# Kernel tuning notes

Measured on AMD Instinct MI355X. Metric: run time of the kernel, lower is better.

## Reference

```python
import jax, jax.numpy as jnp
import numpy as np

N_NODES = 100000
N_EDGES = 1600000
IN_F = 128
HEADS = 4
D_K = 32
OUT_TOTAL = HEADS * D_K


def setup_inputs() -> dict:
    key = jax.random.key(0)
    k1, k2, k3, k4, k5, k6 = jax.random.split(key, 6)
    x = jax.random.normal(k1, (N_NODES, IN_F), dtype=jnp.float32)
    edge_index = jax.random.randint(k2, (2, N_EDGES), 0, N_NODES, dtype=jnp.int64)
    # torch nn.Linear weights: [out, in], xavier-uniform init
    def xavier(k, shape):
        fan_out, fan_in = shape
        lim = float(np.sqrt(6.0 / (fan_in + fan_out)))
        return jax.random.uniform(k, shape, dtype=jnp.float32, minval=-lim, maxval=lim)
    Wq = xavier(k3, (OUT_TOTAL, IN_F))
    Wk = xavier(k4, (OUT_TOTAL, IN_F))
    Wv = xavier(k5, (OUT_TOTAL, IN_F))
    # D init_type='uniform': U(-1, 1)
    D = jax.random.uniform(k6, (HEADS, D_K), dtype=jnp.float32, minval=-1.0, maxval=1.0)
    return {"x": x, "Wq": Wq, "Wk": Wk, "Wv": Wv, "D": D, "edge_index": edge_index}


def reference(x, Wq, Wk, Wv, D, edge_index):
    N = x.shape[0]
    scale = 1.0 / np.sqrt(D_K)
    Q = (x @ Wq.T).reshape(N, HEADS, D_K)
    K = (x @ Wk.T).reshape(N, HEADS, D_K)
    V = (x @ Wv.T).reshape(N, HEADS, D_K)
    row, col = edge_index[0], edge_index[1]
    K_i = K[row]              # [E, H, d]
    Q_j = Q[col]              # [E, H, d]
    diff = K_i - Q_j
    # non-self edges: diff^T diag(D) diff ; self edges: K^T diag(D) Q
    score_edge = jnp.sum(diff * D * diff, axis=-1)          # [E, H]
    score_self = jnp.sum(K_i * D * Q[row], axis=-1)         # [E, H]
    self_mask = (row == col)[:, None]
    scores = jnp.where(self_mask, score_self, score_edge)
    scores = jax.nn.leaky_relu(scores * scale, 0.2)
    # segment softmax over destination node `row`
    smax = jax.ops.segment_max(scores, row, num_segments=N)  # [N, H]
    ex = jnp.exp(scores - smax[row])
    ssum = jax.ops.segment_sum(ex, row, num_segments=N)      # [N, H]
    alpha = ex / (ssum[row] + 1e-16)
    # scatter-add aggregate alpha * V[col] into destination rows
    out = jax.ops.segment_sum(alpha[:, :, None] * V[col], row, num_segments=N)
    return out.reshape(N, OUT_TOTAL)
```

## Files before the change

### kernel.cpp

```cpp
#include <hip/hip_runtime.h>
#include <hip/hip_fp16.h>
#include <cmath>


#define HEADS 4
#define DK 32
#define FDIM 128
#define BINSHIFT 8
#define BINCAP 6144

typedef _Float16 f16x8 __attribute__((ext_vector_type(8)));
typedef float f32x4 __attribute__((ext_vector_type(4)));

__global__ __launch_bounds__(256) void init_buffers(
    int* __restrict__ bin_cursor, int nb)
{
    int gid = blockIdx.x * 256 + threadIdx.x;
    if (gid < nb) bin_cursor[gid] = 0;
}

__global__ __launch_bounds__(256) void split_w(
    const float* __restrict__ Wq, const float* __restrict__ Wk,
    const float* __restrict__ Wv, _Float16* __restrict__ Whf,
    _Float16* __restrict__ Wlf)
{
    const int p = blockIdx.x;
    const float* __restrict__ W = (p == 0) ? Wq : (p == 1 ? Wk : Wv);
#pragma unroll
    for (int i = 0; i < 8; ++i) {
        const int id = i * 256 + threadIdx.x;
        const int g  = id >> 8;
        const int kc = (id >> 6) & 3;
        const int l  = id & 63;
        const int row  = g * 16 + (l & 15);
        const int col0 = kc * 32 + (l >> 4) * 8;
        const float* src = W + row * FDIM + col0;
        const float4 v0 = *reinterpret_cast<const float4*>(src);
        const float4 v1 = *reinterpret_cast<const float4*>(src + 4);
        const float vv[8] = {v0.x, v0.y, v0.z, v0.w, v1.x, v1.y, v1.z, v1.w};
        f16x8 h, lo;
#pragma unroll
        for (int j = 0; j < 8; ++j) {
            _Float16 hh = (_Float16)vv[j];
            h[j]  = hh;
            lo[j] = (_Float16)(vv[j] - (float)hh);
        }
        const size_t off = ((size_t)((p * 8 + g) * 4 + kc) * 64 + l) * 8;
        *reinterpret_cast<f16x8*>(Whf + off) = h;
        *reinterpret_cast<f16x8*>(Wlf + off) = lo;
    }
}

__global__ __launch_bounds__(256) void partition_edges(
    const int* __restrict__ row, const int* __restrict__ col,
    int* __restrict__ bin_cursor, unsigned* __restrict__ pairs,
    int E, int N, int NB)
{
    __shared__ int hist[512];
    __shared__ int basea[512];
    __shared__ int cura[512];
    const int tid = threadIdx.x;
    for (int b = tid; b < 512; b += 256) { hist[b] = 0; cura[b] = 0; }
    __syncthreads();

    const int e0 = blockIdx.x * 4096;
    int rr[16], cc[16];
    if (e0 + 4096 <= E) {
#pragma unroll
        for (int i = 0; i < 4; ++i) {
            const int idx = e0 + i * 1024 + tid * 4;
            const int4 r4 = *reinterpret_cast<const int4*>(row + idx);
            const int4 c4 = *reinterpret_cast<const int4*>(col + idx);
            rr[i*4+0] = r4.x; rr[i*4+1] = r4.y; rr[i*4+2] = r4.z; rr[i*4+3] = r4.w;
            cc[i*4+0] = c4.x; cc[i*4+1] = c4.y; cc[i*4+2] = c4.z; cc[i*4+3] = c4.w;
        }
    } else {
#pragma unroll
        for (int i = 0; i < 4; ++i)
#pragma unroll
            for (int j = 0; j < 4; ++j) {
                const int idx = e0 + i * 1024 + tid * 4 + j;
                rr[i*4+j] = (idx < E) ? row[idx] : -1;
                cc[i*4+j] = (idx < E) ? col[idx] : 0;
            }
    }

#pragma unroll
    for (int i = 0; i < 16; ++i)
        if ((unsigned)rr[i] < (unsigned)N)
            atomicAdd(&hist[rr[i] >> BINSHIFT], 1);
    __syncthreads();

    for (int b = tid; b < NB; b += 256) {
        const int h = hist[b];
        basea[b] = h ? atomicAdd(&bin_cursor[b], h) : 0;
    }
    __syncthreads();

#pragma unroll
    for (int i = 0; i < 16; ++i) {
        const int r = rr[i];
        if ((unsigned)r < (unsigned)N) {
            const int b = r >> BINSHIFT;
            const int p = basea[b] + atomicAdd(&cura[b], 1);
            if (p < BINCAP)
                pairs[(size_t)b * BINCAP + p] =
                    (unsigned)(r & 255) | ((unsigned)cc[i] << 8);
        }
    }
}

__global__ __launch_bounds__(256) void build_csr(
    const int* __restrict__ bin_cursor, const unsigned* __restrict__ pairs,
    int* __restrict__ csr, int* __restrict__ offA, int* __restrict__ cntA,
    int N)
{
    __shared__ int deg[256];
    __shared__ int offs[256];
    __shared__ int cur[256];
    const int b = blockIdx.x;
    const int tid = threadIdx.x;
    deg[tid] = 0;
    __syncthreads();

    int nsize = bin_cursor[b];
    if (nsize > BINCAP) nsize = BINCAP;
    const unsigned* bp = pairs + (size_t)b * BINCAP;

    for (int i = tid; i < nsize; i += 256)
        atomicAdd(&deg[bp[i] & 255], 1);
    __syncthreads();

    const int v = deg[tid];
    offs[tid] = v;
    __syncthreads();
    for (int o = 1; o < 256; o <<= 1) {
        const int t = (tid >= o) ? offs[tid - o] : 0;
        __syncthreads();
        offs[tid] += t;
        __syncthreads();
    }
    const int excl = offs[tid] - v;
    cur[tid] = excl;
    const int node = (b << BINSHIFT) + tid;
    if (node < N) {
        offA[node] = b * BINCAP + excl;
        cntA[node] = v;
    }
    __syncthreads();

    for (int i = tid; i < nsize; i += 256) {
        const unsigned pv = bp[i];
        const int p = atomicAdd(&cur[pv & 255], 1);
        csr[(size_t)b * BINCAP + p] = (int)(pv >> 8);
    }
}

__device__ __forceinline__ int swz_idx(int row, int kk) {
    return (row * FDIM + kk) ^ ((row & 7) << 3);
}

__device__ __forceinline__ void stage_x(
    const float* __restrict__ src, _Float16* __restrict__ dh,
    _Float16* __restrict__ dl, int n0, int nmax, int tid)
{
    const int kk0 = (tid & 15) * 8;
    const int r0  = tid >> 4;
#pragma unroll
    for (int i = 0; i < 4; ++i) {
        const int row = i * 16 + r0;
        float4 v0 = make_float4(0.f, 0.f, 0.f, 0.f), v1 = v0;
        if (n0 + row < nmax) {
            const float* p = src + (size_t)(n0 + row) * FDIM + kk0;
            v0 = *reinterpret_cast<const float4*>(p);
            v1 = *reinterpret_cast<const float4*>(p + 4);
        }
        const float vv[8] = {v0.x, v0.y, v0.z, v0.w, v1.x, v1.y, v1.z, v1.w};
        f16x8 h, l;
#pragma unroll
        for (int j = 0; j < 8; ++j) {
            _Float16 hh = (_Float16)vv[j];
            h[j] = hh;
            l[j] = (_Float16)(vv[j] - (float)hh);
        }
        const int si = swz_idx(row, kk0);
        *reinterpret_cast<f16x8*>(&dh[si]) = h;
        *reinterpret_cast<f16x8*>(&dl[si]) = l;
    }
}

__global__ __launch_bounds__(256) void qkv_gemm(
    const float* __restrict__ x, const _Float16* __restrict__ Whf,
    const _Float16* __restrict__ Wlf, __half* __restrict__ QVh,
    float* __restrict__ Kout, int N)
{
    __shared__ __align__(16) _Float16 xh[64 * 128];
    __shared__ __align__(16) _Float16 xl[64 * 128];

    const int n0  = blockIdx.x * 64;
    const int tid = threadIdx.x;
    const int lane = tid & 63;
    const int wv   = tid >> 6;
    const int wr0  = (wv >> 1) * 32;
    const int wc0  = (wv & 1) * 64;
    const int g0   = wc0 >> 4;
    const int orow = (lane >> 4) * 4;
    const int ocol = lane & 15;

    stage_x(x, xh, xl, n0, N, tid);
    __syncthreads();

    const int lrow = lane & 15;
    const int lk   = (lane >> 4) * 8;

    for (int p = 0; p < 3; ++p) {
        f32x4 acc[2][4];
#pragma unroll
        for (int a = 0; a < 2; ++a)
#pragma unroll
            for (int b = 0; b < 4; ++b)
                acc[a][b] = (f32x4){0.f, 0.f, 0.f, 0.f};

#pragma unroll
        for (int kc = 0; kc < 4; ++kc) {
            f16x8 afh[2], afl[2], bfh[4], bfl[4];
#pragma unroll
            for (int a = 0; a < 2; ++a) {
                const int si = swz_idx(wr0 + a * 16 + lrow, kc * 32 + lk);
                afh[a] = *reinterpret_cast<const f16x8*>(&xh[si]);
                afl[a] = *reinterpret_cast<const f16x8*>(&xl[si]);
            }
#pragma unroll
            for (int b = 0; b < 4; ++b) {
                const size_t off =
                    ((size_t)((p * 8 + g0 + b) * 4 + kc) * 64 + lane) * 8;
                bfh[b] = *reinterpret_cast<const f16x8*>(Whf + off);
                bfl[b] = *reinterpret_cast<const f16x8*>(Wlf + off);
            }
#pragma unroll
            for (int a = 0; a < 2; ++a)
#pragma unroll
                for (int b = 0; b < 4; ++b)
                    acc[a][b] = __builtin_amdgcn_mfma_f32_16x16x32_f16(
                        afh[a], bfh[b], acc[a][b], 0, 0, 0);
#pragma unroll
            for (int a = 0; a < 2; ++a)
#pragma unroll
                for (int b = 0; b < 4; ++b)
                    acc[a][b] = __builtin_amdgcn_mfma_f32_16x16x32_f16(
                        afl[a], bfh[b], acc[a][b], 0, 0, 0);
#pragma unroll
            for (int a = 0; a < 2; ++a)
#pragma unroll
                for (int b = 0; b < 4; ++b)
                    acc[a][b] = __builtin_amdgcn_mfma_f32_16x16x32_f16(
                        afh[a], bfl[b], acc[a][b], 0, 0, 0);
        }

        if (p == 1) {
#pragma unroll
            for (int a = 0; a < 2; ++a) {
#pragma unroll
                for (int r = 0; r < 4; ++r) {
                    const int n = n0 + wr0 + a * 16 + orow + r;
                    if (n < N) {
                        float* op = Kout + (size_t)n * FDIM + wc0 + ocol;
#pragma unroll
                        for (int b = 0; b < 4; ++b)
                            op[b * 16] = acc[a][b][r];
                    }
                }
            }
        } else {
            const int voff = (p == 2) ? 2 : 0;
#pragma unroll
            for (int a = 0; a < 2; ++a) {
#pragma unroll
                for (int r = 0; r < 4; ++r) {
                    const int n = n0 + wr0 + a * 16 + orow + r;
                    if (n < N) {
                        __half* op = QVh + (size_t)n * 256;
#pragma unroll
                        for (int b = 0; b < 4; ++b) {
                            const int d_o = wc0 + ocol + b * 16;
                            op[((d_o >> 1) << 2) + (d_o & 1) + voff] =
                                __float2half(acc[a][b][r]);
                        }
                    }
                }
            }
        }
    }
}

__global__ __launch_bounds__(256) void fused_aggregate(
    const int* __restrict__ offA, const int* __restrict__ cntA,
    const int* __restrict__ csr, const __half* __restrict__ QVh,
    const float* Kb, const float* __restrict__ D, float* out, int N)
{
    int node = blockIdx.x * 4 + (threadIdx.x >> 6);
    if (node >= N) return;
    int lane = threadIdx.x & 63;
    int d = lane * 2;
    const float2 kv = *reinterpret_cast<const float2*>(Kb + (size_t)node * FDIM + d);
    const float D0 = D[d], D1 = D[d + 1];
    const int j0  = offA[node];
    const int cnt = cntA[node];
    float a0 = 0.0f, a1 = 0.0f, se = 0.0f;

    int cc0, cc1, cc2, cc3;
    float2 t0, t1, t2, t3;

#define LOADF(s, idx) { int c_ = __shfl(ec, (idx)); cc##s = c_; \
    t##s = *reinterpret_cast<const float2*>( \
        reinterpret_cast<const __half*>(QVh) + (size_t)c_ * 256 + (lane << 2)); }

#define PROC(s) { \
    float2 qf = __half22float2(*reinterpret_cast<__half2*>(&t##s.x)); \
    float2 vf = __half22float2(*reinterpret_cast<__half2*>(&t##s.y)); \
    float p; \
    if (cc##s == node) { p = D0 * kv.x * qf.x + D1 * kv.y * qf.y; } \
    else { float dx = kv.x - qf.x, dy = kv.y - qf.y; \
           p = D0 * dx * dx + D1 * dy * dy; } \
    p += __shfl_xor(p, 1); p += __shfl_xor(p, 2); \
    p += __shfl_xor(p, 4); p += __shfl_xor(p, 8); \
    float z = p * 0.17677669529663687f; \
    z = fmaxf(z, 0.2f * z); \
    float ex = __expf(z); \
    a0 += ex * vf.x; a1 += ex * vf.y; se += ex; }

    for (int base = 0; base < cnt; base += 64) {
        const int rem = min(64, cnt - base);
        const int ec = (lane < rem) ? csr[j0 + base + lane] : 0;
        int j = 0;
        if (rem >= 4) {
            LOADF(0, 0) LOADF(1, 1) LOADF(2, 2) LOADF(3, 3)
            while (j + 8 <= rem) {
                PROC(0) LOADF(0, j + 4)
                PROC(1) LOADF(1, j + 5)
                PROC(2) LOADF(2, j + 6)
                PROC(3) LOADF(3, j + 7)
                j += 4;
            }
            PROC(0) PROC(1) PROC(2) PROC(3)
            j += 4;
        }
        for (; j < rem; ++j) {
            LOADF(0, j)
            PROC(0)
        }
    }
#undef LOADF
#undef PROC

    float inv = 1.0f / (se + 1e-16f);
    *reinterpret_cast<float2*>(out + (size_t)node * FDIM + d) =
        make_float2(a0 * inv, a1 * inv);
}

extern "C" void kernel_launch(void* const* d_in, const int* in_sizes, int n_in,
                              void* d_out, int out_size, void* d_ws, size_t ws_size,
                              hipStream_t stream) {
    const float* x  = (const float*)d_in[0];
    const float* Wq = (const float*)d_in[1];
    const float* Wk = (const float*)d_in[2];
    const float* Wv = (const float*)d_in[3];
    const float* D  = (const float*)d_in[4];
    const int*  edge = (const int*)d_in[5];
    float* out = (float*)d_out;

    const int N = in_sizes[0] / FDIM;
    const int E = in_sizes[5] / 2;
    const int* row = edge;
    const int* col = edge + E;

    const int NB = (N + 255) >> 8;

    __half* QVh = (__half*)d_ws;
    unsigned* pairs = (unsigned*)(QVh + (size_t)N * 256);
    int* csr  = (int*)(pairs + (size_t)NB * BINCAP);
    int* offA = csr + (size_t)NB * BINCAP;
    int* cntA = offA + N;
    int* bin_cursor = cntA + N;
    _Float16* Whf = (_Float16*)(bin_cursor + 512);
    _Float16* Wlf = Whf + 3 * 16384;
    float* Kout = out;

    init_buffers<<<(NB + 255) / 256, 256, 0, stream>>>(bin_cursor, NB);
    split_w<<<3, 256, 0, stream>>>(Wq, Wk, Wv, Whf, Wlf);

    partition_edges<<<(E + 4095) / 4096, 256, 0, stream>>>(
        row, col, bin_cursor, pairs, E, N, NB);
    build_csr<<<NB, 256, 0, stream>>>(
        bin_cursor, pairs, csr, offA, cntA, N);

    qkv_gemm<<<(N + 63) / 64, 256, 0, stream>>>(
        x, Whf, Wlf, QVh, Kout, N);

    fused_aggregate<<<(N + 3) / 4, 256, 0, stream>>>(
        offA, cntA, csr, QVh, Kout, D, out, N);
}
```

Measured before the change: 314.5 us.

## Process two edges per wave with 16-byte QV gathers in aggregation

The fp16 Q/V buffer is re-interleaved in groups of four dims, so each lane loads 4 Q plus 4 V values in one 16-byte load. Each half-wave now handles a separate edge, so a wave covers two edges per step, and the two halves' accumulators are merged at the end. The CSR now stores precomputed byte offsets (node<<9) to save address arithmetic. The head reduction drops to three shuffles, and an odd trailing edge is split half-weight across both halves. Separately, the tiny init_buffers kernel is folded into split_w to save a launch.

```diff
diff --git a/kernel.cpp b/kernel.cpp
--- a/kernel.cpp
+++ b/kernel.cpp
@@ -12,18 +12,14 @@
 typedef _Float16 f16x8 __attribute__((ext_vector_type(8)));
 typedef float f32x4 __attribute__((ext_vector_type(4)));
 
-__global__ __launch_bounds__(256) void init_buffers(
-    int* __restrict__ bin_cursor, int nb)
-{
-    int gid = blockIdx.x * 256 + threadIdx.x;
-    if (gid < nb) bin_cursor[gid] = 0;
-}
-
 __global__ __launch_bounds__(256) void split_w(
     const float* __restrict__ Wq, const float* __restrict__ Wk,
     const float* __restrict__ Wv, _Float16* __restrict__ Whf,
-    _Float16* __restrict__ Wlf)
-{
+    _Float16* __restrict__ Wlf, int* __restrict__ bin_cursor, int nb)
+{
+    const int gid = blockIdx.x * 256 + threadIdx.x;
+    if (gid < nb) bin_cursor[gid] = 0;
+
     const int p = blockIdx.x;
     const float* __restrict__ W = (p == 0) ? Wq : (p == 1 ? Wk : Wv);
 #pragma unroll
@@ -152,7 +148,7 @@
     for (int i = tid; i < nsize; i += 256) {
         const unsigned pv = bp[i];
         const int p = atomicAdd(&cur[pv & 255], 1);
-        csr[(size_t)b * BINCAP + p] = (int)(pv >> 8);
+        csr[(size_t)b * BINCAP + p] = (int)((pv >> 8) << 9);
     }
 }
 
@@ -272,7 +268,7 @@
                 }
             }
         } else {
-            const int voff = (p == 2) ? 2 : 0;
+            const int voff = (p == 2) ? 4 : 0;
 #pragma unroll
             for (int a = 0; a < 2; ++a) {
 #pragma unroll
@@ -283,7 +279,7 @@
 #pragma unroll
                         for (int b = 0; b < 4; ++b) {
                             const int d_o = wc0 + ocol + b * 16;
-                            op[((d_o >> 1) << 2) + (d_o & 1) + voff] =
+                            op[((d_o >> 2) << 3) + (d_o & 3) + voff] =
                                 __float2half(acc[a][b][r]);
                         }
                     }
@@ -300,62 +296,101 @@
 {
     int node = blockIdx.x * 4 + (threadIdx.x >> 6);
     if (node >= N) return;
-    int lane = threadIdx.x & 63;
-    int d = lane * 2;
-    const float2 kv = *reinterpret_cast<const float2*>(Kb + (size_t)node * FDIM + d);
-    const float D0 = D[d], D1 = D[d + 1];
+    const int lane = threadIdx.x & 63;
+    const int hl   = lane & 31;
+    const int side = lane >> 5;
+    const int d0   = hl << 2;
+    const float4 kv = *reinterpret_cast<const float4*>(Kb + (size_t)node * FDIM + d0);
+    const float4 Dv = *reinterpret_cast<const float4*>(D + d0);
+    const float Dk0 = Dv.x * kv.x, Dk1 = Dv.y * kv.y,
+                Dk2 = Dv.z * kv.z, Dk3 = Dv.w * kv.w;
     const int j0  = offA[node];
     const int cnt = cntA[node];
-    float a0 = 0.0f, a1 = 0.0f, se = 0.0f;
+    const int nb  = node << 9;
+    float a0 = 0.f, a1 = 0.f, a2 = 0.f, a3 = 0.f, se = 0.f;
 
     int cc0, cc1, cc2, cc3;
-    float2 t0, t1, t2, t3;
-
-#define LOADF(s, idx) { int c_ = __shfl(ec, (idx)); cc##s = c_; \
-    t##s = *reinterpret_cast<const float2*>( \
-        reinterpret_cast<const __half*>(QVh) + (size_t)c_ * 256 + (lane << 2)); }
-
-#define PROC(s) { \
-    float2 qf = __half22float2(*reinterpret_cast<__half2*>(&t##s.x)); \
-    float2 vf = __half22float2(*reinterpret_cast<__half2*>(&t##s.y)); \
+    float4 t0, t1, t2, t3;
+
+#define LOADP(s, p) { int c_ = __shfl(ecb, 2 * (p) + side); cc##s = c_; \
+    t##s = *reinterpret_cast<const float4*>( \
+        reinterpret_cast<const char*>(QVh) + (size_t)(unsigned)c_ + (hl << 4)); }
+
+#define PROCP(s) { \
+    const __half2* th = reinterpret_cast<const __half2*>(&t##s); \
+    float2 q01 = __half22float2(th[0]); float2 q23 = __half22float2(th[1]); \
+    float2 v01 = __half22float2(th[2]); float2 v23 = __half22float2(th[3]); \
     float p; \
-    if (cc##s == node) { p = D0 * kv.x * qf.x + D1 * kv.y * qf.y; } \
-    else { float dx = kv.x - qf.x, dy = kv.y - qf.y; \
-           p = D0 * dx * dx + D1 * dy * dy; } \
-    p += __shfl_xor(p, 1); p += __shfl_xor(p, 2); \
-    p += __shfl_xor(p, 4); p += __shfl_xor(p, 8); \
+    if (cc##s == nb) { \
+        p = Dk0 * q01.x + Dk1 * q01.y + Dk2 * q23.x + Dk3 * q23.y; \
+    } else { \
+        float e0 = kv.x - q01.x, e1 = kv.y - q01.y; \
+        float e2 = kv.z - q23.x, e3 = kv.w - q23.y; \
+        p = Dv.x*e0*e0 + Dv.y*e1*e1 + Dv.z*e2*e2 + Dv.w*e3*e3; \
+    } \
+    p += __shfl_xor(p, 1); p += __shfl_xor(p, 2); p += __shfl_xor(p, 4); \
     float z = p * 0.17677669529663687f; \
     z = fmaxf(z, 0.2f * z); \
     float ex = __expf(z); \
-    a0 += ex * vf.x; a1 += ex * vf.y; se += ex; }
+    a0 += ex * v01.x; a1 += ex * v01.y; \
+    a2 += ex * v23.x; a3 += ex * v23.y; se += ex; }
 
     for (int base = 0; base < cnt; base += 64) {
         const int rem = min(64, cnt - base);
-        const int ec = (lane < rem) ? csr[j0 + base + lane] : 0;
-        int j = 0;
-        if (rem >= 4) {
-            LOADF(0, 0) LOADF(1, 1) LOADF(2, 2) LOADF(3, 3)
-            while (j + 8 <= rem) {
-                PROC(0) LOADF(0, j + 4)
-                PROC(1) LOADF(1, j + 5)
-                PROC(2) LOADF(2, j + 6)
-                PROC(3) LOADF(3, j + 7)
-                j += 4;
-            }
-            PROC(0) PROC(1) PROC(2) PROC(3)
-            j += 4;
-        }
-        for (; j < rem; ++j) {
-            LOADF(0, j)
-            PROC(0)
-        }
-    }
-#undef LOADF
-#undef PROC
-
-    float inv = 1.0f / (se + 1e-16f);
-    *reinterpret_cast<float2*>(out + (size_t)node * FDIM + d) =
-        make_float2(a0 * inv, a1 * inv);
+        const int ecb = (lane < rem) ? csr[j0 + base + lane] : 0;
+        const int npair = rem >> 1;
+        int pj = 0;
+        if (npair >= 4) {
+            LOADP(0, 0) LOADP(1, 1) LOADP(2, 2) LOADP(3, 3)
+            while (pj + 8 <= npair) {
+                PROCP(0) LOADP(0, pj + 4)
+                PROCP(1) LOADP(1, pj + 5)
+                PROCP(2) LOADP(2, pj + 6)
+                PROCP(3) LOADP(3, pj + 7)
+                pj += 4;
+            }
+            PROCP(0) PROCP(1) PROCP(2) PROCP(3)
+            pj += 4;
+        }
+        for (; pj < npair; ++pj) {
+            LOADP(0, pj)
+            PROCP(0)
+        }
+        if (rem & 1) {
+            const int c_ = __shfl(ecb, rem - 1);
+            float4 tt = *reinterpret_cast<const float4*>(
+                reinterpret_cast<const char*>(QVh) + (size_t)(unsigned)c_ + (hl << 4));
+            const __half2* th = reinterpret_cast<const __half2*>(&tt);
+            float2 q01 = __half22float2(th[0]); float2 q23 = __half22float2(th[1]);
+            float2 v01 = __half22float2(th[2]); float2 v23 = __half22float2(th[3]);
+            float p;
+            if (c_ == nb) {
+                p = Dk0 * q01.x + Dk1 * q01.y + Dk2 * q23.x + Dk3 * q23.y;
+            } else {
+                float e0 = kv.x - q01.x, e1 = kv.y - q01.y;
+                float e2 = kv.z - q23.x, e3 = kv.w - q23.y;
+                p = Dv.x*e0*e0 + Dv.y*e1*e1 + Dv.z*e2*e2 + Dv.w*e3*e3;
+            }
+            p += __shfl_xor(p, 1); p += __shfl_xor(p, 2); p += __shfl_xor(p, 4);
+            float z = p * 0.17677669529663687f;
+            z = fmaxf(z, 0.2f * z);
+            float ex = __expf(z) * 0.5f;
+            a0 += ex * v01.x; a1 += ex * v01.y;
+            a2 += ex * v23.x; a3 += ex * v23.y; se += ex;
+        }
+    }
+#undef LOADP
+#undef PROCP
+
+    a0 += __shfl_xor(a0, 32); a1 += __shfl_xor(a1, 32);
+    a2 += __shfl_xor(a2, 32); a3 += __shfl_xor(a3, 32);
+    se += __shfl_xor(se, 32);
+
+    if (side == 0) {
+        const float inv = 1.0f / (se + 1e-16f);
+        *reinterpret_cast<float4*>(out + (size_t)node * FDIM + d0) =
+            make_float4(a0 * inv, a1 * inv, a2 * inv, a3 * inv);
+    }
 }
 
 extern "C" void kernel_launch(void* const* d_in, const int* in_sizes, int n_in,
@@ -386,8 +421,7 @@
     _Float16* Wlf = Whf + 3 * 16384;
     float* Kout = out;
 
-    init_buffers<<<(NB + 255) / 256, 256, 0, stream>>>(bin_cursor, NB);
-    split_w<<<3, 256, 0, stream>>>(Wq, Wk, Wv, Whf, Wlf);
+    split_w<<<3, 256, 0, stream>>>(Wq, Wk, Wv, Whf, Wlf, bin_cursor, NB);
 
     partition_edges<<<(E + 4095) / 4096, 256, 0, stream>>>(
         row, col, bin_cursor, pairs, E, N, NB);
```

Result: no change. 313.2 us (-0.4%).
